# Kernel optimization log

Hardware: AMD Instinct MI355X
Metric: run time of the kernel (lower is better)

## Reference

```python
import jax, jax.numpy as jnp
import numpy as np

K = 1024   # number of NNLS components (theta_1 is K x K)
B = 8192   # batched frames / columns


def setup_inputs() -> dict:
    key = jax.random.key(0)
    k1, k2, k3, k4 = jax.random.split(key, 4)
    # theta_1 = I - AtA / ||AtA||_F  -> near-identity contraction; emulate with
    # identity minus a small random symmetric-ish perturbation.
    pert = jax.random.normal(k1, (K, K), dtype=jnp.float32) * (1.0 / K)
    th1 = jnp.eye(K, dtype=jnp.float32) - pert
    Y = jax.random.uniform(k2, (K, B), dtype=jnp.float32)
    X_old = jax.random.uniform(k3, (K, B), dtype=jnp.float32)
    weight = jax.random.normal(k4, (K, B), dtype=jnp.float32) * 0.1  # theta_2 = Atb/n_AtA
    k = 2  # PGD iteration counter
    return {"th1": th1, "Y": Y, "X_old": X_old, "k": k, "weight": weight}


def reference(th1, Y, X_old, k, weight):
    # One projected-gradient-descent step of NNLS with Nesterov momentum:
    #   new_X = relu(th1 @ Y + weight)
    #   Y_new = new_X + (k-1)/(k+2) * (new_X - X_old)
    kf = jnp.float32(k)
    new_X = jax.nn.relu(jnp.matmul(th1, Y) + weight)          # [K, B]
    momentum = (kf - 1.0) / (kf + 2.0)
    Y_new = new_X + momentum * (new_X - X_old)                # [K, B]
    return (Y_new, new_X, k + 1, weight)
```

## Files before the change

### kernel.cpp

```cpp
#include <hip/hip_runtime.h>
#include <cstdint>


#define KDIM 1024
#define NDIM 8192
#define KB_ELEMS (1024UL * 8192UL)

typedef short short8 __attribute__((ext_vector_type(8)));
typedef float f32x4 __attribute__((ext_vector_type(4)));

__device__ __forceinline__ uint32_t pk2(float a, float b) {
  uint32_t ua = __builtin_bit_cast(uint32_t, a) + 0x8000u;
  uint32_t ub = __builtin_bit_cast(uint32_t, b) + 0x8000u;
  return (ua >> 16) | (ub & 0xFFFF0000u);
}

__global__ __launch_bounds__(256, 2) void nnls_gemm(
    const float* __restrict__ th1, const float* __restrict__ Y,
    const float* __restrict__ xold, const int* __restrict__ kin,
    const float* __restrict__ weight, float* __restrict__ out)
{
  __shared__ __align__(16) unsigned short As[128 * 32];
  __shared__ __align__(16) unsigned short Bs[128 * 32];

  const int tid  = threadIdx.x;
  const int lane = tid & 63;
  const int w    = tid >> 6;
  const int wm = w >> 1, wn = w & 1;
  const int quad = lane >> 4, nl = lane & 15;

  const int m0 = blockIdx.y * 128;
  const int n0 = blockIdx.x * 128;

  const int nn = 2 * lane;
  const int ks = w * 8;
  const float* ybase = Y + (size_t)ks * NDIM + n0 + nn;

  const int ar = tid >> 3;
  const int ac = tid & 7;
  const float* abase = th1 + (size_t)(m0 + ar) * KDIM + ac * 4;

  float2 yb[8];
  float4 ab[4];
#pragma unroll
  for (int r = 0; r < 8; ++r) yb[r] = *(const float2*)(ybase + (size_t)r * NDIM);
#pragma unroll
  for (int g = 0; g < 4; ++g) ab[g] = *(const float4*)(abase + (size_t)(32 * g) * KDIM);

  f32x4 acc[4][4] = {};

  for (int kt = 0; kt < 32; ++kt) {
#pragma unroll
    for (int g = 0; g < 4; ++g) {
      uint2 d;
      d.x = pk2(ab[g].x, ab[g].y);
      d.y = pk2(ab[g].z, ab[g].w);
      *(uint2*)&As[(ar + 32 * g) * 32 + ac * 4] = d;
    }
#pragma unroll
    for (int j = 0; j < 2; ++j) {
      const int n  = nn + j;
      const int ch = w ^ ((n >> 3) & 3);
      uint4 d;
      d.x = pk2(j ? yb[0].y : yb[0].x, j ? yb[1].y : yb[1].x);
      d.y = pk2(j ? yb[2].y : yb[2].x, j ? yb[3].y : yb[3].x);
      d.z = pk2(j ? yb[4].y : yb[4].x, j ? yb[5].y : yb[5].x);
      d.w = pk2(j ? yb[6].y : yb[6].x, j ? yb[7].y : yb[7].x);
      *(uint4*)&Bs[n * 32 + ch * 8] = d;
    }
    __syncthreads();

    if (kt < 31) {
      const float* yn = ybase + (size_t)((kt + 1) * 32) * NDIM;
      const float* an = abase + (kt + 1) * 32;
#pragma unroll
      for (int r = 0; r < 8; ++r) yb[r] = *(const float2*)(yn + (size_t)r * NDIM);
#pragma unroll
      for (int g = 0; g < 4; ++g) ab[g] = *(const float4*)(an + (size_t)(32 * g) * KDIM);
    }

    short8 af[4], bf[4];
#pragma unroll
    for (int i = 0; i < 4; ++i) {
      af[i] = *(const short8*)&As[(wm * 64 + i * 16 + nl) * 32 + quad * 8];
      const int n  = wn * 64 + i * 16 + nl;
      const int ch = quad ^ ((n >> 3) & 3);
      bf[i] = *(const short8*)&Bs[n * 32 + ch * 8];
    }
#pragma unroll
    for (int i = 0; i < 4; ++i)
#pragma unroll
      for (int j = 0; j < 4; ++j)
        acc[i][j] = __builtin_amdgcn_mfma_f32_16x16x32_bf16(af[i], bf[j], acc[i][j], 0, 0, 0);

    __syncthreads();
  }

  const float kf  = (float)kin[0];
  const float mom = (kf - 1.0f) / (kf + 2.0f);
#pragma unroll
  for (int i = 0; i < 4; ++i) {
#pragma unroll
    for (int j = 0; j < 4; ++j) {
      const int mbase = m0 + wm * 64 + i * 16 + quad * 4;
      const int nidx  = n0 + wn * 64 + j * 16 + nl;
#pragma unroll
      for (int r = 0; r < 4; ++r) {
        const size_t idx = (size_t)(mbase + r) * NDIM + nidx;
        const float wv = weight[idx];
        const float xo = xold[idx];
        const float nx = fmaxf(acc[i][j][r] + wv, 0.0f);
        const float yn = nx + mom * (nx - xo);
        out[idx] = yn;
        out[KB_ELEMS + idx] = nx;
        out[2 * KB_ELEMS + 1 + idx] = wv;
      }
    }
  }

  if (blockIdx.x == 0 && blockIdx.y == 0 && tid == 0) {
    out[2 * KB_ELEMS] = (float)(kin[0] + 1);
  }
}

extern "C" void kernel_launch(void* const* d_in, const int* in_sizes, int n_in,
                              void* d_out, int out_size, void* d_ws, size_t ws_size,
                              hipStream_t stream) {
  const float* th1  = (const float*)d_in[0];
  const float* Y    = (const float*)d_in[1];
  const float* xold = (const float*)d_in[2];
  const int*   kin  = (const int*)d_in[3];
  const float* wgt  = (const float*)d_in[4];
  float* out = (float*)d_out;

  dim3 grid(NDIM / 128, KDIM / 128);
  nnls_gemm<<<grid, 256, 0, stream>>>(th1, Y, xold, kin, wgt, out);
}
```

Before: 247.5 us.

## Use 512-thread blocks, padded LDS tiles, and an LDS-staged vectorized epilogue

Doubles the threads per block to 512 (8 waves), so each wave owns a 32x64 output tile instead of 64x64. The B tile now uses a padded LDS layout (stride 40) in place of the XOR swizzle. The epilogue stages accumulators through swizzled LDS so that weight/xold loads and the three output stores become float4-vectorized and row-contiguous, where before they were scattered scalar accesses. In exchange it adds LDS round-trips and extra barriers in the epilogue, and issues more scalar Y loads per thread.

```diff
diff --git a/kernel.cpp b/kernel.cpp
--- a/kernel.cpp
+++ b/kernel.cpp
@@ -5,9 +5,12 @@
 #define KDIM 1024
 #define NDIM 8192
 #define KB_ELEMS (1024UL * 8192UL)
+#define LDA 40
 
 typedef short short8 __attribute__((ext_vector_type(8)));
 typedef float f32x4 __attribute__((ext_vector_type(4)));
+
+struct __attribute__((aligned(4))) f4u { float x, y, z, w; };
 
 __device__ __forceinline__ uint32_t pk2(float a, float b) {
   uint32_t ua = __builtin_bit_cast(uint32_t, a) + 0x8000u;
@@ -15,13 +18,14 @@
   return (ua >> 16) | (ub & 0xFFFF0000u);
 }
 
-__global__ __launch_bounds__(256, 2) void nnls_gemm(
+__global__ __launch_bounds__(512, 4) void nnls_gemm(
     const float* __restrict__ th1, const float* __restrict__ Y,
     const float* __restrict__ xold, const int* __restrict__ kin,
     const float* __restrict__ weight, float* __restrict__ out)
 {
-  __shared__ __align__(16) unsigned short As[128 * 32];
-  __shared__ __align__(16) unsigned short Bs[128 * 32];
+  __shared__ __align__(16) char smem[32768];
+  unsigned short* As = (unsigned short*)smem;
+  unsigned short* Bs = (unsigned short*)(smem + 10240);
 
   const int tid  = threadIdx.x;
   const int lane = tid & 63;
@@ -32,63 +36,54 @@
   const int m0 = blockIdx.y * 128;
   const int n0 = blockIdx.x * 128;
 
-  const int nn = 2 * lane;
-  const int ks = w * 8;
-  const float* ybase = Y + (size_t)ks * NDIM + n0 + nn;
-
   const int ar = tid >> 3;
   const int ac = tid & 7;
   const float* abase = th1 + (size_t)(m0 + ar) * KDIM + ac * 4;
 
-  float2 yb[8];
-  float4 ab[4];
+  const int bn = tid & 127;
+  const int bk = (tid >> 7) * 8;
+  const float* ybase = Y + (size_t)bk * NDIM + n0 + bn;
+
+  float4 ab[2];
+  float  yb[8];
+  ab[0] = *(const float4*)(abase);
+  ab[1] = *(const float4*)(abase + (size_t)64 * KDIM);
 #pragma unroll
-  for (int r = 0; r < 8; ++r) yb[r] = *(const float2*)(ybase + (size_t)r * NDIM);
-#pragma unroll
-  for (int g = 0; g < 4; ++g) ab[g] = *(const float4*)(abase + (size_t)(32 * g) * KDIM);
+  for (int r = 0; r < 8; ++r) yb[r] = ybase[(size_t)r * NDIM];
 
-  f32x4 acc[4][4] = {};
+  f32x4 acc[2][4] = {};
 
   for (int kt = 0; kt < 32; ++kt) {
-#pragma unroll
-    for (int g = 0; g < 4; ++g) {
-      uint2 d;
-      d.x = pk2(ab[g].x, ab[g].y);
-      d.y = pk2(ab[g].z, ab[g].w);
-      *(uint2*)&As[(ar + 32 * g) * 32 + ac * 4] = d;
-    }
-#pragma unroll
-    for (int j = 0; j < 2; ++j) {
-      const int n  = nn + j;
-      const int ch = w ^ ((n >> 3) & 3);
-      uint4 d;
-      d.x = pk2(j ? yb[0].y : yb[0].x, j ? yb[1].y : yb[1].x);
-      d.y = pk2(j ? yb[2].y : yb[2].x, j ? yb[3].y : yb[3].x);
-      d.z = pk2(j ? yb[4].y : yb[4].x, j ? yb[5].y : yb[5].x);
-      d.w = pk2(j ? yb[6].y : yb[6].x, j ? yb[7].y : yb[7].x);
-      *(uint4*)&Bs[n * 32 + ch * 8] = d;
+    {
+      uint2 d0; d0.x = pk2(ab[0].x, ab[0].y); d0.y = pk2(ab[0].z, ab[0].w);
+      *(uint2*)&As[ar * LDA + ac * 4] = d0;
+      uint2 d1; d1.x = pk2(ab[1].x, ab[1].y); d1.y = pk2(ab[1].z, ab[1].w);
+      *(uint2*)&As[(ar + 64) * LDA + ac * 4] = d1;
+      uint4 e;
+      e.x = pk2(yb[0], yb[1]); e.y = pk2(yb[2], yb[3]);
+      e.z = pk2(yb[4], yb[5]); e.w = pk2(yb[6], yb[7]);
+      *(uint4*)&Bs[bn * LDA + bk] = e;
     }
     __syncthreads();
 
     if (kt < 31) {
+      const float* an = abase + (kt + 1) * 32;
+      ab[0] = *(const float4*)(an);
+      ab[1] = *(const float4*)(an + (size_t)64 * KDIM);
       const float* yn = ybase + (size_t)((kt + 1) * 32) * NDIM;
-      const float* an = abase + (kt + 1) * 32;
 #pragma unroll
-      for (int r = 0; r < 8; ++r) yb[r] = *(const float2*)(yn + (size_t)r * NDIM);
-#pragma unroll
-      for (int g = 0; g < 4; ++g) ab[g] = *(const float4*)(an + (size_t)(32 * g) * KDIM);
+      for (int r = 0; r < 8; ++r) yb[r] = yn[(size_t)r * NDIM];
     }
 
-    short8 af[4], bf[4];
+    short8 af[2], bf[4];
 #pragma unroll
-    for (int i = 0; i < 4; ++i) {
-      af[i] = *(const short8*)&As[(wm * 64 + i * 16 + nl) * 32 + quad * 8];
-      const int n  = wn * 64 + i * 16 + nl;
-      const int ch = quad ^ ((n >> 3) & 3);
-      bf[i] = *(const short8*)&Bs[n * 32 + ch * 8];
-    }
+    for (int i = 0; i < 2; ++i)
+      af[i] = *(const short8*)&As[(wm * 32 + i * 16 + nl) * LDA + quad * 8];
 #pragma unroll
-    for (int i = 0; i < 4; ++i)
+    for (int j = 0; j < 4; ++j)
+      bf[j] = *(const short8*)&Bs[(wn * 64 + j * 16 + nl) * LDA + quad * 8];
+#pragma unroll
+    for (int i = 0; i < 2; ++i)
 #pragma unroll
       for (int j = 0; j < 4; ++j)
         acc[i][j] = __builtin_amdgcn_mfma_f32_16x16x32_bf16(af[i], bf[j], acc[i][j], 0, 0, 0);
@@ -98,29 +93,47 @@
 
   const float kf  = (float)kin[0];
   const float mom = (kf - 1.0f) / (kf + 2.0f);
+  float* ep = (float*)smem + w * 1024;
+  const int lr = lane >> 2;
+  const int cb = (lane & 3) * 16;
+  const int swzR = 16 * ((lr >> 2) & 1) + 4 * (lr & 3);
+
 #pragma unroll
-  for (int i = 0; i < 4; ++i) {
+  for (int i = 0; i < 2; ++i) {
 #pragma unroll
-    for (int j = 0; j < 4; ++j) {
-      const int mbase = m0 + wm * 64 + i * 16 + quad * 4;
-      const int nidx  = n0 + wn * 64 + j * 16 + nl;
+    for (int j = 0; j < 4; ++j)
 #pragma unroll
       for (int r = 0; r < 4; ++r) {
-        const size_t idx = (size_t)(mbase + r) * NDIM + nidx;
-        const float wv = weight[idx];
-        const float xo = xold[idx];
-        const float nx = fmaxf(acc[i][j][r] + wv, 0.0f);
-        const float yn = nx + mom * (nx - xo);
-        out[idx] = yn;
-        out[KB_ELEMS + idx] = nx;
-        out[2 * KB_ELEMS + 1 + idx] = wv;
+        const int wrow = quad * 4 + r;
+        const int colp = (j * 16 + nl) ^ (16 * (quad & 1) + 4 * r);
+        ep[wrow * 64 + colp] = acc[i][j][r];
       }
+    __syncthreads();
+
+    const int mg = m0 + wm * 32 + i * 16 + lr;
+#pragma unroll
+    for (int t = 0; t < 4; ++t) {
+      const int colp = (cb + 4 * t) ^ swzR;
+      const float4 cv = *(const float4*)&ep[lr * 64 + colp];
+      const int ng = n0 + wn * 64 + cb + 4 * t;
+      const size_t idx = (size_t)mg * NDIM + ng;
+      const float4 wv = *(const float4*)&weight[idx];
+      const float4 xo = *(const float4*)&xold[idx];
+      float4 nx, yn;
+      nx.x = fmaxf(cv.x + wv.x, 0.0f); nx.y = fmaxf(cv.y + wv.y, 0.0f);
+      nx.z = fmaxf(cv.z + wv.z, 0.0f); nx.w = fmaxf(cv.w + wv.w, 0.0f);
+      yn.x = nx.x + mom * (nx.x - xo.x); yn.y = nx.y + mom * (nx.y - xo.y);
+      yn.z = nx.z + mom * (nx.z - xo.z); yn.w = nx.w + mom * (nx.w - xo.w);
+      *(float4*)&out[idx] = yn;
+      *(float4*)&out[KB_ELEMS + idx] = nx;
+      f4u s; s.x = wv.x; s.y = wv.y; s.z = wv.z; s.w = wv.w;
+      *(f4u*)&out[2 * KB_ELEMS + 1 + idx] = s;
     }
+    __syncthreads();
   }
 
-  if (blockIdx.x == 0 && blockIdx.y == 0 && tid == 0) {
+  if (blockIdx.x == 0 && blockIdx.y == 0 && tid == 0)
     out[2 * KB_ELEMS] = (float)(kin[0] + 1);
-  }
 }
 
 extern "C" void kernel_launch(void* const* d_in, const int* in_sizes, int n_in,
@@ -134,5 +147,5 @@
   float* out = (float*)d_out;
 
   dim3 grid(NDIM / 128, KDIM / 128);
-  nnls_gemm<<<grid, 256, 0, stream>>>(th1, Y, xold, kin, wgt, out);
+  nnls_gemm<<<grid, 512, 0, stream>>>(th1, Y, xold, kin, wgt, out);
 }
```

Result: faster. 239.5 us (-3.2%).
